# Kernel tuning notes

Hardware: AMD Instinct MI355X
Metric: run time of the kernel (lower is better)

The kernel has to match this reference:

```python
import jax, jax.numpy as jnp
import numpy as np

GRID_RANGE = ((-3.0, 3.0), (-3.0, 3.0))
GRID_SHAPE = (64, 64)
INIT_LENGTHSCALE = 0.1


def _construct_grid():
    axes = [jnp.linspace(lo, hi, s, dtype=jnp.float32)
            for (lo, hi), s in zip(GRID_RANGE, GRID_SHAPE)]
    mesh = jnp.meshgrid(*axes, indexing='ij')
    return jnp.stack(mesh, axis=-1)  # [64, 64, dx]


def setup_inputs() -> dict:
    key = jax.random.key(0)
    k1, k2 = jax.random.split(key)
    m, n, dx, dz = 8, 4096, 2, 16
    x = jax.random.normal(k1, (m, n, dx), dtype=jnp.float32)
    z = jax.random.normal(k2, (m, n, dz), dtype=jnp.float32)
    # lengthscale_param = log(exp(init_lengthscale) - 1), per dim
    ls_param = jnp.log(jnp.expm1(jnp.full((dx,), INIT_LENGTHSCALE, dtype=jnp.float32)))
    grid = _construct_grid()
    return {"x": x, "z": z, "lengthscale_param": ls_param, "grid": grid}


def reference(x, z, lengthscale_param, grid):
    # lengthscale = 1e-5 + softplus(param), per input dim
    ls = 1e-5 + jax.nn.softplus(lengthscale_param)  # [dx]
    m = x.shape[0]
    grid_flat = grid.reshape(-1, grid.shape[-1])  # [M, dx]
    # per-dim scaled differences; sum((g-x)^2 / ls^2) == sum(((g-x)/ls)^2)
    diff = (grid_flat[None, :, None, :] - x[:, None, :, :]) / ls  # [m, M, n, dx]
    pre_exp = jnp.sum(diff * diff, axis=-1)                        # [m, M, n]
    weights = jnp.exp(-0.5 * pre_exp)                              # [m, M, n]
    z_grid_flat = jnp.einsum('bmn,bnd->bmd', weights, z)           # [m, M, dz]
    z_grid = z_grid_flat.reshape((m,) + grid.shape[:-1] + (z.shape[-1],))
    x_grid = jnp.broadcast_to(grid[None], (m,) + grid.shape)
    return (x_grid, z_grid)
```

## Files before the change

### kernel.cpp

```cpp
#include <hip/hip_runtime.h>
#include <hip/hip_bf16.h>
#include <cstdint>

#define N_PTS   4096
#define M_GRID  4096
#define LOG2E   1.4426950408889634f
#define SKIP_E0L (-28.853900817779268f)

typedef __attribute__((ext_vector_type(8))) short  short8;
typedef __attribute__((ext_vector_type(4))) float  floatx4;

#define OFF_EX   0
#define OFF_NN   32768
#define OFF_CNT  40960
#define SMEM_BYTES 40964

__device__ __forceinline__ uint32_t pack_bf2(float a, float b) {
    union { __hip_bfloat162 h; uint32_t u; } c;
    c.h = __float22bfloat162_rn(make_float2(a, b));
    return c.u;
}

__global__ __launch_bounds__(512, 4)
void setconv_kernel(const float2* __restrict__ x2,
                    const float*  __restrict__ zf,
                    const float*  __restrict__ lsp,
                    const float2* __restrict__ grid2,
                    float2*       __restrict__ outx,
                    float*        __restrict__ outz)
{
    __shared__ __align__(16) char smem[SMEM_BYTES];
    float2*  ex   = reinterpret_cast<float2*>(smem + OFF_EX);
    ushort*  nn   = reinterpret_cast<ushort*>(smem + OFF_NN);
    int*     cntp = reinterpret_cast<int*>(smem + OFF_CNT);
    floatx4* redv = reinterpret_cast<floatx4*>(smem);

    const int tid  = threadIdx.x;
    const int lane = tid & 63;
    const int w    = tid >> 6;
    const int mt   = w & 3;
    const int ks   = w >> 2;
    const int q    = lane >> 4;
    const int dn   = lane & 15;
    const int b    = blockIdx.y;
    const int gtile = (int)((blockIdx.x + ((b & 4) ? 32u : 0u)) & 63u);

    float p0 = lsp[0], p1 = lsp[1];
    float sp0 = (p0 > 0.f) ? (p0 + log1pf(expf(-p0))) : log1pf(expf(p0));
    float sp1 = (p1 > 0.f) ? (p1 + log1pf(expf(-p1))) : log1pf(expf(p1));
    float ls0 = 1e-5f + sp0, ls1 = 1e-5f + sp1;
    const float q0L = -0.5f * LOG2E / (ls0 * ls0);
    const float q1L = -0.5f * LOG2E / (ls1 * ls1);

    const float2 gv = grid2[gtile * 64 + lane];
    const float  g0 = gv.x;
    if (w == 0) outx[(size_t)b * M_GRID + gtile * 64 + lane] = gv;
    const float g1m = grid2[gtile * 64 + mt * 16 + dn].y;

    if (tid == 0) *cntp = 0;
    __syncthreads();

    const float2* xb = x2 + b * N_PTS;

    for (int t = tid; t < N_PTS; t += 512) {
        float2 xv = xb[t];
        float d0 = g0 - xv.x;
        float e0 = q0L * d0 * d0;
        bool keep = (e0 >= SKIP_E0L);
        unsigned long long m = __ballot(keep);
        int base = 0;
        if (lane == 0 && m) base = atomicAdd(cntp, __popcll(m));
        base = __shfl(base, 0);
        if (keep) {
            int off = base + __popcll(m & ((1ull << lane) - 1ull));
            ex[off] = make_float2(e0, xv.y);
            nn[off] = (ushort)(t << 4);
        }
    }
    __syncthreads();
    const int C    = *cntp;
    const int Cpad = (C + 63) & ~63;
    for (int t = C + tid; t < Cpad; t += 512) {
        ex[t] = make_float2(-1e30f, 0.f);
        nn[t] = 0;
    }
    __syncthreads();

    const int ngroup = Cpad >> 6;
    const float* zb = zf + (size_t)b * (N_PTS * 16);

    floatx4 acc = {0.f, 0.f, 0.f, 0.f};

    if (ngroup > 0) {
        const float4* e4 = reinterpret_cast<const float4*>(ex);

        float4 A, B, Cc, D; uint4 N;
        float a0, a1, a2, a3, a4, a5, a6, a7;

#define LDREC(gi, A_, B_, C_, D_, N_) do {                                  \
        int k0_ = ((gi) << 6) + (ks << 5) + (q << 3);                       \
        int h_  = k0_ >> 1;                                                 \
        A_ = e4[h_]; B_ = e4[h_ + 1]; C_ = e4[h_ + 2]; D_ = e4[h_ + 3];     \
        N_ = *reinterpret_cast<const uint4*>(nn + k0_);                     \
    } while (0)

#define LDZ(N_) do {                                                        \
        a0 = zb[(int)((N_).x & 0xffffu) + dn];                              \
        a1 = zb[(int)((N_).x >> 16)     + dn];                              \
        a2 = zb[(int)((N_).y & 0xffffu) + dn];                              \
        a3 = zb[(int)((N_).y >> 16)     + dn];                              \
        a4 = zb[(int)((N_).z & 0xffffu) + dn];                              \
        a5 = zb[(int)((N_).z >> 16)     + dn];                              \
        a6 = zb[(int)((N_).w & 0xffffu) + dn];                              \
        a7 = zb[(int)((N_).w >> 16)     + dn];                              \
    } while (0)

        LDREC(0, A, B, Cc, D, N);
        LDZ(N);

        for (int gi = 0; gi < ngroup; ++gi) {
            const int nx = (gi + 1 < ngroup) ? gi + 1 : gi;
            float4 A2, B2, C2, D2; uint4 N2;
            LDREC(nx, A2, B2, C2, D2, N2);

            float u0 = g1m - A.y,  u1 = g1m - A.w;
            float u2 = g1m - B.y,  u3 = g1m - B.w;
            float u4 = g1m - Cc.y, u5 = g1m - Cc.w;
            float u6 = g1m - D.y,  u7 = g1m - D.w;
            float w0 = exp2f(fmaf(q1L * u0, u0, A.x));
            float w1 = exp2f(fmaf(q1L * u1, u1, A.z));
            float w2 = exp2f(fmaf(q1L * u2, u2, B.x));
            float w3 = exp2f(fmaf(q1L * u3, u3, B.z));
            float w4 = exp2f(fmaf(q1L * u4, u4, Cc.x));
            float w5 = exp2f(fmaf(q1L * u5, u5, Cc.z));
            float w6 = exp2f(fmaf(q1L * u6, u6, D.x));
            float w7 = exp2f(fmaf(q1L * u7, u7, D.z));

            union { uint32_t u[4]; short8 s; } af, bf;
            af.u[0] = pack_bf2(w0, w1); af.u[1] = pack_bf2(w2, w3);
            af.u[2] = pack_bf2(w4, w5); af.u[3] = pack_bf2(w6, w7);
            bf.u[0] = pack_bf2(a0, a1); bf.u[1] = pack_bf2(a2, a3);
            bf.u[2] = pack_bf2(a4, a5); bf.u[3] = pack_bf2(a6, a7);

            acc = __builtin_amdgcn_mfma_f32_16x16x32_bf16(af.s, bf.s, acc, 0, 0, 0);

            LDZ(N2);
            A = A2; B = B2; Cc = C2; D = D2;
        }
#undef LDREC
#undef LDZ
    }

    __syncthreads();
    if (w >= 4) redv[(w - 4) * 64 + lane] = acc;
    __syncthreads();
    if (w < 4) {
        acc += redv[mt * 64 + lane];
        size_t base = ((size_t)b * M_GRID + gtile * 64 + mt * 16 + q * 4) * 16 + dn;
#pragma unroll
        for (int r = 0; r < 4; ++r)
            outz[base + (size_t)r * 16] = acc[r];
    }
}

extern "C" void kernel_launch(void* const* d_in, const int* in_sizes, int n_in,
                              void* d_out, int out_size, void* d_ws, size_t ws_size,
                              hipStream_t stream) {
    const float2* x2    = (const float2*)d_in[0];
    const float*  zf    = (const float*)d_in[1];
    const float*  lsp   = (const float*)d_in[2];
    const float2* grid2 = (const float2*)d_in[3];
    float* out = (float*)d_out;

    hipLaunchKernelGGL(setconv_kernel, dim3(64, 8), dim3(512), 0, stream,
                       x2, zf, lsp, grid2, (float2*)out, out + 65536);
}
```

Measured before the change: 83.41 us.

## Tighten skip threshold, vectorize x loads, deepen gather prefetch

```diff
diff --git a/kernel.cpp b/kernel.cpp
--- a/kernel.cpp
+++ b/kernel.cpp
@@ -5,7 +5,7 @@
 #define N_PTS   4096
 #define M_GRID  4096
 #define LOG2E   1.4426950408889634f
-#define SKIP_E0L (-28.853900817779268f)
+#define SKIP_E0L (-20.197730572445487f)
 
 typedef __attribute__((ext_vector_type(8))) short  short8;
 typedef __attribute__((ext_vector_type(4))) float  floatx4;
@@ -20,6 +20,8 @@
     c.h = __float22bfloat162_rn(make_float2(a, b));
     return c.u;
 }
+
+struct Rec { float4 a, b, c, d; uint4 n; };
 
 __global__ __launch_bounds__(512, 4)
 void setconv_kernel(const float2* __restrict__ x2,
@@ -60,21 +62,25 @@
     if (tid == 0) *cntp = 0;
     __syncthreads();
 
-    const float2* xb = x2 + b * N_PTS;
-
-    for (int t = tid; t < N_PTS; t += 512) {
-        float2 xv = xb[t];
-        float d0 = g0 - xv.x;
-        float e0 = q0L * d0 * d0;
-        bool keep = (e0 >= SKIP_E0L);
-        unsigned long long m = __ballot(keep);
-        int base = 0;
-        if (lane == 0 && m) base = atomicAdd(cntp, __popcll(m));
-        base = __shfl(base, 0);
-        if (keep) {
-            int off = base + __popcll(m & ((1ull << lane) - 1ull));
-            ex[off] = make_float2(e0, xv.y);
-            nn[off] = (ushort)(t << 4);
+    const float4* xb4 = reinterpret_cast<const float4*>(x2 + b * N_PTS);
+    for (int tt = tid; tt < N_PTS / 2; tt += 512) {
+        float4 xv = xb4[tt];
+#pragma unroll
+        for (int h = 0; h < 2; ++h) {
+            float x0 = h ? xv.z : xv.x;
+            float x1 = h ? xv.w : xv.y;
+            float d0 = g0 - x0;
+            float e0 = q0L * d0 * d0;
+            bool keep = (e0 >= SKIP_E0L);
+            unsigned long long m = __ballot(keep);
+            int base = 0;
+            if (lane == 0 && m) base = atomicAdd(cntp, __popcll(m));
+            base = __shfl(base, 0);
+            if (keep) {
+                int off = base + __popcll(m & ((1ull << lane) - 1ull));
+                ex[off] = make_float2(e0, x1);
+                nn[off] = (ushort)((2 * tt + h) << 4);
+            }
         }
     }
     __syncthreads();
@@ -93,62 +99,61 @@
 
     if (ngroup > 0) {
         const float4* e4 = reinterpret_cast<const float4*>(ex);
+        const int kofs = (ks << 5) + (q << 3);
 
-        float4 A, B, Cc, D; uint4 N;
-        float a0, a1, a2, a3, a4, a5, a6, a7;
+        auto ldrec = [&](int gi) {
+            Rec r;
+            int k0 = (gi << 6) + kofs;
+            int h  = k0 >> 1;
+            r.a = e4[h]; r.b = e4[h + 1]; r.c = e4[h + 2]; r.d = e4[h + 3];
+            r.n = *reinterpret_cast<const uint4*>(nn + k0);
+            return r;
+        };
 
-#define LDREC(gi, A_, B_, C_, D_, N_) do {                                  \
-        int k0_ = ((gi) << 6) + (ks << 5) + (q << 3);                       \
-        int h_  = k0_ >> 1;                                                 \
-        A_ = e4[h_]; B_ = e4[h_ + 1]; C_ = e4[h_ + 2]; D_ = e4[h_ + 3];     \
-        N_ = *reinterpret_cast<const uint4*>(nn + k0_);                     \
-    } while (0)
-
-#define LDZ(N_) do {                                                        \
-        a0 = zb[(int)((N_).x & 0xffffu) + dn];                              \
-        a1 = zb[(int)((N_).x >> 16)     + dn];                              \
-        a2 = zb[(int)((N_).y & 0xffffu) + dn];                              \
-        a3 = zb[(int)((N_).y >> 16)     + dn];                              \
-        a4 = zb[(int)((N_).z & 0xffffu) + dn];                              \
-        a5 = zb[(int)((N_).z >> 16)     + dn];                              \
-        a6 = zb[(int)((N_).w & 0xffffu) + dn];                              \
-        a7 = zb[(int)((N_).w >> 16)     + dn];                              \
-    } while (0)
-
-        LDREC(0, A, B, Cc, D, N);
-        LDZ(N);
+        Rec rc = ldrec(0);
+        Rec rn = ldrec(ngroup > 1 ? 1 : 0);
+        float zc[8], zn[8];
+#pragma unroll
+        for (int j = 0; j < 8; ++j) {
+            uint32_t nv = (&rc.n.x)[j >> 1];
+            zc[j] = zb[(int)((j & 1) ? (nv >> 16) : (nv & 0xffffu)) + dn];
+        }
 
         for (int gi = 0; gi < ngroup; ++gi) {
-            const int nx = (gi + 1 < ngroup) ? gi + 1 : gi;
-            float4 A2, B2, C2, D2; uint4 N2;
-            LDREC(nx, A2, B2, C2, D2, N2);
+            if (gi + 1 < ngroup) {
+#pragma unroll
+                for (int j = 0; j < 8; ++j) {
+                    uint32_t nv = (&rn.n.x)[j >> 1];
+                    zn[j] = zb[(int)((j & 1) ? (nv >> 16) : (nv & 0xffffu)) + dn];
+                }
+            }
+            Rec r2 = ldrec(gi + 2 < ngroup ? gi + 2 : ngroup - 1);
 
-            float u0 = g1m - A.y,  u1 = g1m - A.w;
-            float u2 = g1m - B.y,  u3 = g1m - B.w;
-            float u4 = g1m - Cc.y, u5 = g1m - Cc.w;
-            float u6 = g1m - D.y,  u7 = g1m - D.w;
-            float w0 = exp2f(fmaf(q1L * u0, u0, A.x));
-            float w1 = exp2f(fmaf(q1L * u1, u1, A.z));
-            float w2 = exp2f(fmaf(q1L * u2, u2, B.x));
-            float w3 = exp2f(fmaf(q1L * u3, u3, B.z));
-            float w4 = exp2f(fmaf(q1L * u4, u4, Cc.x));
-            float w5 = exp2f(fmaf(q1L * u5, u5, Cc.z));
-            float w6 = exp2f(fmaf(q1L * u6, u6, D.x));
-            float w7 = exp2f(fmaf(q1L * u7, u7, D.z));
+            float u0 = g1m - rc.a.y, u1 = g1m - rc.a.w;
+            float u2 = g1m - rc.b.y, u3 = g1m - rc.b.w;
+            float u4 = g1m - rc.c.y, u5 = g1m - rc.c.w;
+            float u6 = g1m - rc.d.y, u7 = g1m - rc.d.w;
+            float w0 = exp2f(fmaf(q1L * u0, u0, rc.a.x));
+            float w1 = exp2f(fmaf(q1L * u1, u1, rc.a.z));
+            float w2 = exp2f(fmaf(q1L * u2, u2, rc.b.x));
+            float w3 = exp2f(fmaf(q1L * u3, u3, rc.b.z));
+            float w4 = exp2f(fmaf(q1L * u4, u4, rc.c.x));
+            float w5 = exp2f(fmaf(q1L * u5, u5, rc.c.z));
+            float w6 = exp2f(fmaf(q1L * u6, u6, rc.d.x));
+            float w7 = exp2f(fmaf(q1L * u7, u7, rc.d.z));
 
             union { uint32_t u[4]; short8 s; } af, bf;
-            af.u[0] = pack_bf2(w0, w1); af.u[1] = pack_bf2(w2, w3);
-            af.u[2] = pack_bf2(w4, w5); af.u[3] = pack_bf2(w6, w7);
-            bf.u[0] = pack_bf2(a0, a1); bf.u[1] = pack_bf2(a2, a3);
-            bf.u[2] = pack_bf2(a4, a5); bf.u[3] = pack_bf2(a6, a7);
+            af.u[0] = pack_bf2(w0, w1);     af.u[1] = pack_bf2(w2, w3);
+            af.u[2] = pack_bf2(w4, w5);     af.u[3] = pack_bf2(w6, w7);
+            bf.u[0] = pack_bf2(zc[0], zc[1]); bf.u[1] = pack_bf2(zc[2], zc[3]);
+            bf.u[2] = pack_bf2(zc[4], zc[5]); bf.u[3] = pack_bf2(zc[6], zc[7]);
 
             acc = __builtin_amdgcn_mfma_f32_16x16x32_bf16(af.s, bf.s, acc, 0, 0, 0);
 
-            LDZ(N2);
-            A = A2; B = B2; Cc = C2; D = D2;
+            rc = rn; rn = r2;
+#pragma unroll
+            for (int j = 0; j < 8; ++j) zc[j] = zn[j];
         }
-#undef LDREC
-#undef LDZ
     }
 
     __syncthreads();
```

After: 81.73 us. -2.0%, faster.
